# Kernel optimization log

Measured on AMD Instinct MI355X. Metric: run time of the kernel, lower is better.

## Reference

```python
import jax, jax.numpy as jnp
import numpy as np

NUM_HEADS = 8
NUM_GROUPS = 32
EPS = 1e-5


def setup_inputs() -> dict:
    key = jax.random.key(0)
    ks = jax.random.split(key, 7)
    B, C, H, W = 8, 512, 32, 32
    x = jax.random.normal(ks[0], (B, C, H, W), dtype=jnp.float32)
    # GroupNorm affine params
    gn_w = jnp.ones((C,), dtype=jnp.float32)
    gn_b = jnp.zeros((C,), dtype=jnp.float32)
    # 1x1 conv == linear over channel dim; store squeezed weights (out, in)
    qkv_w = jax.random.normal(ks[1], (3 * C, C), dtype=jnp.float32) * (1.0 / np.sqrt(C))
    qkv_b = jnp.zeros((3 * C,), dtype=jnp.float32)
    proj_w = jax.random.normal(ks[2], (C, C), dtype=jnp.float32) * (1.0 / np.sqrt(C))
    proj_b = jnp.zeros((C,), dtype=jnp.float32)
    return {"x": x, "gn_w": gn_w, "gn_b": gn_b, "qkv_w": qkv_w,
            "qkv_b": qkv_b, "proj_w": proj_w, "proj_b": proj_b}


def reference(x, gn_w, gn_b, qkv_w, qkv_b, proj_w, proj_b):
    B, C, H, W = x.shape
    G = NUM_GROUPS
    hd = C // NUM_HEADS
    scale = hd ** -0.5
    # GroupNorm: normalize over (C//G, H, W) per group
    xg = x.reshape(B, G, C // G, H, W)
    mean = xg.mean(axis=(2, 3, 4), keepdims=True)
    var = xg.var(axis=(2, 3, 4), keepdims=True)
    xn = ((xg - mean) * jax.lax.rsqrt(var + EPS)).reshape(B, C, H, W)
    xn = xn * gn_w[None, :, None, None] + gn_b[None, :, None, None]
    # QKV 1x1 conv
    qkv = jnp.einsum('bchw,oc->bohw', xn, qkv_w) + qkv_b[None, :, None, None]
    # (B, 3, heads, head_dim, HW) -> (3, B, heads, HW, head_dim)
    qkv = qkv.reshape(B, 3, NUM_HEADS, hd, H * W).transpose(1, 0, 2, 4, 3)
    q, k, v = qkv[0], qkv[1], qkv[2]
    attn = jax.nn.softmax(jnp.einsum('bhqd,bhkd->bhqk', q, k) * scale, axis=-1)
    out = jnp.einsum('bhqk,bhkd->bhqd', attn, v)  # (B, heads, HW, hd)
    out = out.transpose(0, 1, 3, 2).reshape(B, C, H, W)
    out = jnp.einsum('bchw,oc->bohw', out, proj_w) + proj_b[None, :, None, None]
    return out + x
```

## Files before the change

### kernel.cpp

```cpp
#include <hip/hip_runtime.h>
#include <hip/hip_bf16.h>
#include <math.h>

typedef __bf16 bf16_t;
typedef __bf16 bf16x8 __attribute__((ext_vector_type(8)));
typedef __bf16 bf16x4 __attribute__((ext_vector_type(4)));
typedef float  f32x4  __attribute__((ext_vector_type(4)));

#define NB    8
#define NC    512
#define NHW   1024
#define NHEAD 8
#define NHD   64
#define NG    32
#define NCG   16
#define NO3   1536

__device__ __forceinline__ void lds_load16(bf16_t* lds, const bf16_t* g) {
  __builtin_amdgcn_global_load_lds(
      (__attribute__((address_space(1))) unsigned int*)(g),
      (__attribute__((address_space(3))) unsigned int*)(void*)(lds),
      16, 0, 0);
}

__device__ __forceinline__ float sum16(float v) {
  v += __shfl_xor(v, 1); v += __shfl_xor(v, 2);
  v += __shfl_xor(v, 4); v += __shfl_xor(v, 8);
  return v;
}
__device__ __forceinline__ float max16(float v) {
  v = fmaxf(v, __shfl_xor(v, 1)); v = fmaxf(v, __shfl_xor(v, 2));
  v = fmaxf(v, __shfl_xor(v, 4)); v = fmaxf(v, __shfl_xor(v, 8));
  return v;
}

__global__ __launch_bounds__(256)
void gn_kernel(const float* __restrict__ x, const float* __restrict__ gw,
               const float* __restrict__ gb, bf16_t* __restrict__ xn)
{
  const int bg = blockIdx.x;
  const int b = bg >> 5, g = bg & 31;
  const float* xp = x + ((size_t)b * NC + g * NCG) * NHW;
  const int tid = threadIdx.x;
  const int wave = tid >> 6, lane = tid & 63;

  float s1 = 0.f, s2 = 0.f;
  const float4* xp4 = (const float4*)xp;
  for (int i = tid; i < 4096; i += 256) {
    float4 v = xp4[i];
    s1 += v.x + v.y + v.z + v.w;
    s2 += v.x * v.x + v.y * v.y + v.z * v.z + v.w * v.w;
  }
  for (int off = 32; off > 0; off >>= 1) {
    s1 += __shfl_down(s1, off);
    s2 += __shfl_down(s2, off);
  }
  __shared__ float red[16];
  if (lane == 0) { red[wave] = s1; red[8 + wave] = s2; }
  __syncthreads();
  float tot1 = red[0] + red[1] + red[2] + red[3];
  float tot2 = red[8] + red[9] + red[10] + red[11];
  const float mean = tot1 * (1.0f / 16384.0f);
  const float var  = tot2 * (1.0f / 16384.0f) - mean * mean;
  const float rstd = rsqrtf(var + 1e-5f);

  float gam[NCG], bet[NCG];
  #pragma unroll
  for (int c = 0; c < NCG; ++c) {
    gam[c] = gw[g * NCG + c] * rstd;
    bet[c] = gb[g * NCG + c] - mean * gam[c];
  }
  bf16_t* op = xn + (size_t)b * NHW * NC + g * NCG;
  for (int s = tid; s < NHW; s += 256) {
    __align__(16) bf16_t vals[NCG];
    #pragma unroll
    for (int c = 0; c < NCG; ++c)
      vals[c] = (bf16_t)(xp[c * NHW + s] * gam[c] + bet[c]);
    *(bf16x8*)(op + (size_t)s * NC)     = *(const bf16x8*)&vals[0];
    *(bf16x8*)(op + (size_t)s * NC + 8) = *(const bf16x8*)&vals[8];
  }
}

__global__ __launch_bounds__(256)
void wconv_kernel(const float* __restrict__ qw, const float* __restrict__ pw,
                  bf16_t* __restrict__ qwb, bf16_t* __restrict__ pwb)
{
  const int gid = blockIdx.x * 256 + threadIdx.x;
  const int n1 = NO3 * NC / 4;
  float4 v; bf16x4 o;
  if (gid < n1) {
    v = ((const float4*)qw)[gid];
    o[0] = (bf16_t)v.x; o[1] = (bf16_t)v.y; o[2] = (bf16_t)v.z; o[3] = (bf16_t)v.w;
    ((bf16x4*)qwb)[gid] = o;
  } else {
    int g2 = gid - n1;
    v = ((const float4*)pw)[g2];
    o[0] = (bf16_t)v.x; o[1] = (bf16_t)v.y; o[2] = (bf16_t)v.z; o[3] = (bf16_t)v.w;
    ((bf16x4*)pwb)[g2] = o;
  }
}

__device__ __forceinline__ void gemm_mainloop(const bf16_t* Ap, const bf16_t* Bp,
                                              bf16_t* sA, bf16_t* sB, f32x4 (&acc)[4][4])
{
  const int tid = threadIdx.x;
  const int wave = tid >> 6, lane = tid & 63;
  const int quad = lane >> 4, l16 = lane & 15;
  const int wm = wave >> 1, wn = wave & 1;
  for (int k0 = 0; k0 < 512; k0 += 32) {
    #pragma unroll
    for (int j = 0; j < 2; ++j) {
      int c = wave * 64 + j * 256 + lane;
      int row = c >> 2, ko = (c & 3) * 8;
      lds_load16(sA + (size_t)(wave * 64 + j * 256) * 8, Ap + (size_t)row * 512 + k0 + ko);
      lds_load16(sB + (size_t)(wave * 64 + j * 256) * 8, Bp + (size_t)row * 512 + k0 + ko);
    }
    __syncthreads();
    bf16x8 af[4], bfr[4];
    #pragma unroll
    for (int mi = 0; mi < 4; ++mi)
      af[mi] = *(const bf16x8*)(sA + (wm * 64 + mi * 16 + l16) * 32 + quad * 8);
    #pragma unroll
    for (int ni = 0; ni < 4; ++ni)
      bfr[ni] = *(const bf16x8*)(sB + (wn * 64 + ni * 16 + l16) * 32 + quad * 8);
    #pragma unroll
    for (int mi = 0; mi < 4; ++mi)
      #pragma unroll
      for (int ni = 0; ni < 4; ++ni)
        acc[mi][ni] = __builtin_amdgcn_mfma_f32_16x16x32_bf16(af[mi], bfr[ni], acc[mi][ni], 0, 0, 0);
    __syncthreads();
  }
}

__global__ __launch_bounds__(256, 2)
void qkv_gemm(const bf16_t* __restrict__ xn, const bf16_t* __restrict__ w,
              const float* __restrict__ bias,
              bf16_t* __restrict__ qbuf, bf16_t* __restrict__ kbuf, bf16_t* __restrict__ vbuf)
{
  __shared__ __align__(16) bf16_t smem[128 * 136];
  bf16_t* sA = smem;
  bf16_t* sB = smem + 4096;
  const int tid = threadIdx.x;
  const int wave = tid >> 6, lane = tid & 63;
  const int quad = lane >> 4, l16 = lane & 15;
  const int wm = wave >> 1, wn = wave & 1;
  const int bx = blockIdx.x, by = blockIdx.y, b = blockIdx.z;

  const bf16_t* Ap = xn + ((size_t)b * NHW + by * 128) * NC;
  const bf16_t* Bp = w + (size_t)bx * 128 * NC;
  f32x4 acc[4][4] = {};
  gemm_mainloop(Ap, Bp, sA, sB, acc);

  const int obase = bx * 128 + wn * 64;
  const int sbase = by * 128 + wm * 64;
  float bv[4];
  #pragma unroll
  for (int ni = 0; ni < 4; ++ni) bv[ni] = bias[obase + ni * 16 + l16];

  if (bx < 8) {
    const bool isq = (bx < 4);
    bf16_t* basep = isq ? qbuf : kbuf;
    const float scale = isq ? 0.125f : 1.0f;
    #pragma unroll
    for (int ni = 0; ni < 4; ++ni) {
      int o = obase + ni * 16 + l16;
      int hh = (o >> 6) & 7, dd = o & 63;
      bf16_t* dst = basep + ((size_t)(b * NHEAD + hh) * NHW) * NHD + dd;
      #pragma unroll
      for (int mi = 0; mi < 4; ++mi)
        #pragma unroll
        for (int r = 0; r < 4; ++r) {
          int s = sbase + mi * 16 + quad * 4 + r;
          dst[(size_t)s * NHD] = (bf16_t)((acc[mi][ni][r] + bv[ni]) * scale);
        }
    }
  } else {
    bf16_t* sC = smem;
    #pragma unroll
    for (int ni = 0; ni < 4; ++ni)
      #pragma unroll
      for (int mi = 0; mi < 4; ++mi)
        #pragma unroll
        for (int r = 0; r < 4; ++r)
          sC[(wn * 64 + ni * 16 + l16) * 136 + wm * 64 + mi * 16 + quad * 4 + r] =
              (bf16_t)(acc[mi][ni][r] + bv[ni]);
    __syncthreads();
    int o_local = tid >> 1, shalf = (tid & 1) << 6;
    int ov = (bx - 8) * 128 + o_local;
    int hh = ov >> 6, dd = ov & 63;
    bf16_t* dst = vbuf + ((size_t)(b * NHEAD + hh) * NHD + dd) * NHW + by * 128 + shalf;
    #pragma unroll
    for (int jj = 0; jj < 8; ++jj)
      *(bf16x8*)(dst + jj * 8) = *(const bf16x8*)&sC[o_local * 136 + shalf + jj * 8];
  }
}

__global__ __launch_bounds__(256, 2)
void attn_kernel(const bf16_t* __restrict__ qbuf, const bf16_t* __restrict__ kbuf,
                 const bf16_t* __restrict__ vbuf, bf16_t* __restrict__ obuf)
{
  __shared__ __align__(16) bf16_t Ks[128 * 72];
  __shared__ __align__(16) bf16_t Vs[64 * 136];
  __shared__ __align__(16) bf16_t Ps[4][32 * 136];

  const int tid = threadIdx.x;
  const int wave = tid >> 6, lane = tid & 63;
  const int quad = lane >> 4, l16 = lane & 15;
  const int idx = blockIdx.x;
  const int qt = idx & 7, h = (idx >> 3) & 7, b = idx >> 6;
  const size_t bh = (size_t)b * NHEAD + h;
  const bf16_t* qp = qbuf + (bh * NHW + qt * 128) * NHD;
  const bf16_t* kp = kbuf + bh * NHW * NHD;
  const bf16_t* vp = vbuf + bh * NHD * NHW;

  bf16x8 qf[2][2];
  #pragma unroll
  for (int mi = 0; mi < 2; ++mi)
    #pragma unroll
    for (int kc = 0; kc < 2; ++kc)
      qf[mi][kc] = *(const bf16x8*)(qp + (size_t)(wave * 32 + mi * 16 + l16) * NHD + kc * 32 + quad * 8);

  float m_i[2][4], l_i[2][4];
  f32x4 oacc[2][4] = {};
  #pragma unroll
  for (int mi = 0; mi < 2; ++mi)
    #pragma unroll
    for (int r = 0; r < 4; ++r) { m_i[mi][r] = -1e30f; l_i[mi][r] = 0.f; }

  for (int kt = 0; kt < 8; ++kt) {
    const bf16_t* ksrc = kp + (size_t)kt * 128 * NHD;
    const bf16_t* vsrc = vp + kt * 128;
    #pragma unroll
    for (int j = 0; j < 4; ++j) {
      int c = tid + j * 256;
      int t = c >> 3, doff = (c & 7) * 8;
      *(bf16x8*)&Ks[t * 72 + doff] = *(const bf16x8*)(ksrc + (size_t)t * NHD + doff);
    }
    #pragma unroll
    for (int j = 0; j < 4; ++j) {
      int c = tid + j * 256;
      int d = c >> 4, toff = (c & 15) * 8;
      *(bf16x8*)&Vs[d * 136 + toff] = *(const bf16x8*)(vsrc + (size_t)d * NHW + toff);
    }
    __syncthreads();

    f32x4 sf[2][8] = {};
    #pragma unroll
    for (int ni = 0; ni < 8; ++ni) {
      bf16x8 k0 = *(const bf16x8*)&Ks[(ni * 16 + l16) * 72 + quad * 8];
      bf16x8 k1 = *(const bf16x8*)&Ks[(ni * 16 + l16) * 72 + 32 + quad * 8];
      #pragma unroll
      for (int mi = 0; mi < 2; ++mi) {
        sf[mi][ni] = __builtin_amdgcn_mfma_f32_16x16x32_bf16(qf[mi][0], k0, sf[mi][ni], 0, 0, 0);
        sf[mi][ni] = __builtin_amdgcn_mfma_f32_16x16x32_bf16(qf[mi][1], k1, sf[mi][ni], 0, 0, 0);
      }
    }
    float alpha[2][4], rs[2][4];
    #pragma unroll
    for (int mi = 0; mi < 2; ++mi)
      #pragma unroll
      for (int r = 0; r < 4; ++r) {
        float mx = sf[mi][0][r];
        #pragma unroll
        for (int ni = 1; ni < 8; ++ni) mx = fmaxf(mx, sf[mi][ni][r]);
        mx = max16(mx);
        float mnew = fmaxf(m_i[mi][r], mx);
        alpha[mi][r] = __expf(m_i[mi][r] - mnew);
        m_i[mi][r] = mnew;
        rs[mi][r] = 0.f;
      }
    #pragma unroll
    for (int mi = 0; mi < 2; ++mi)
      #pragma unroll
      for (int ni = 0; ni < 8; ++ni)
        #pragma unroll
        for (int r = 0; r < 4; ++r) {
          float p = __expf(sf[mi][ni][r] - m_i[mi][r]);
          rs[mi][r] += p;
          Ps[wave][(mi * 16 + quad * 4 + r) * 136 + ni * 16 + l16] = (bf16_t)p;
        }
    #pragma unroll
    for (int mi = 0; mi < 2; ++mi)
      #pragma unroll
      for (int r = 0; r < 4; ++r)
        l_i[mi][r] = l_i[mi][r] * alpha[mi][r] + sum16(rs[mi][r]);
    #pragma unroll
    for (int mi = 0; mi < 2; ++mi)
      #pragma unroll
      for (int ni = 0; ni < 4; ++ni)
        #pragma unroll
        for (int r = 0; r < 4; ++r)
          oacc[mi][ni][r] *= alpha[mi][r];

    asm volatile("s_waitcnt lgkmcnt(0)" ::: "memory");

    #pragma unroll
    for (int kc = 0; kc < 4; ++kc) {
      bf16x8 pa0 = *(const bf16x8*)&Ps[wave][(l16) * 136 + kc * 32 + quad * 8];
      bf16x8 pa1 = *(const bf16x8*)&Ps[wave][(16 + l16) * 136 + kc * 32 + quad * 8];
      #pragma unroll
      for (int ni = 0; ni < 4; ++ni) {
        bf16x8 vf = *(const bf16x8*)&Vs[(ni * 16 + l16) * 136 + kc * 32 + quad * 8];
        oacc[0][ni] = __builtin_amdgcn_mfma_f32_16x16x32_bf16(pa0, vf, oacc[0][ni], 0, 0, 0);
        oacc[1][ni] = __builtin_amdgcn_mfma_f32_16x16x32_bf16(pa1, vf, oacc[1][ni], 0, 0, 0);
      }
    }
    __syncthreads();
  }

  #pragma unroll
  for (int mi = 0; mi < 2; ++mi)
    #pragma unroll
    for (int r = 0; r < 4; ++r) {
      float inv = 1.0f / l_i[mi][r];
      int s = qt * 128 + wave * 32 + mi * 16 + quad * 4 + r;
      bf16_t* orow = obuf + ((size_t)b * NHW + s) * NC + h * NHD;
      #pragma unroll
      for (int ni = 0; ni < 4; ++ni)
        orow[ni * 16 + l16] = (bf16_t)(oacc[mi][ni][r] * inv);
    }
}

__global__ __launch_bounds__(256, 2)
void proj_gemm(const bf16_t* __restrict__ ob, const bf16_t* __restrict__ w,
               const float* __restrict__ bias, const float* __restrict__ x,
               float* __restrict__ out)
{
  __shared__ __align__(16) bf16_t smem[8192];
  bf16_t* sA = smem;
  bf16_t* sB = smem + 4096;
  const int tid = threadIdx.x;
  const int wave = tid >> 6, lane = tid & 63;
  const int quad = lane >> 4, l16 = lane & 15;
  const int wm = wave >> 1, wn = wave & 1;
  const int bx = blockIdx.x, by = blockIdx.y, b = blockIdx.z;

  const bf16_t* Ap = w + (size_t)by * 128 * NC;
  const bf16_t* Bp = ob + ((size_t)b * NHW + bx * 128) * NC;
  f32x4 acc[4][4] = {};
  gemm_mainloop(Ap, Bp, sA, sB, acc);

  const int cobase = by * 128 + wm * 64;
  const int sbase  = bx * 128 + wn * 64;
  #pragma unroll
  for (int mi = 0; mi < 4; ++mi)
    #pragma unroll
    for (int r = 0; r < 4; ++r) {
      int co = cobase + mi * 16 + quad * 4 + r;
      float pb = bias[co];
      const float* xrow = x + ((size_t)b * NC + co) * NHW;
      float* orow = out + ((size_t)b * NC + co) * NHW;
      #pragma unroll
      for (int ni = 0; ni < 4; ++ni) {
        int s = sbase + ni * 16 + l16;
        orow[s] = acc[mi][ni][r] + pb + xrow[s];
      }
    }
}

extern "C" void kernel_launch(void* const* d_in, const int* in_sizes, int n_in,
                              void* d_out, int out_size, void* d_ws, size_t ws_size,
                              hipStream_t stream)
{
  const float* x      = (const float*)d_in[0];
  const float* gn_w   = (const float*)d_in[1];
  const float* gn_b   = (const float*)d_in[2];
  const float* qkv_w  = (const float*)d_in[3];
  const float* qkv_b  = (const float*)d_in[4];
  const float* proj_w = (const float*)d_in[5];
  const float* proj_b = (const float*)d_in[6];
  float* out = (float*)d_out;

  char* ws = (char*)d_ws;
  bf16_t* xn   = (bf16_t*)(ws);
  bf16_t* qwb  = (bf16_t*)(ws + 8388608);
  bf16_t* pwb  = (bf16_t*)(ws + 9961472);
  bf16_t* qbuf = (bf16_t*)(ws + 10485760);
  bf16_t* kbuf = (bf16_t*)(ws + 18874368);
  bf16_t* vbuf = (bf16_t*)(ws + 27262976);
  bf16_t* obuf = xn;

  gn_kernel<<<dim3(NB * NG), dim3(256), 0, stream>>>(x, gn_w, gn_b, xn);
  wconv_kernel<<<dim3(1024), dim3(256), 0, stream>>>(qkv_w, proj_w, qwb, pwb);
  qkv_gemm<<<dim3(12, 8, NB), dim3(256), 0, stream>>>(xn, qwb, qkv_b, qbuf, kbuf, vbuf);
  attn_kernel<<<dim3(512), dim3(256), 0, stream>>>(qbuf, kbuf, vbuf, obuf);
  proj_gemm<<<dim3(8, 4, NB), dim3(256), 0, stream>>>(obuf, pwb, proj_b, x, out);
}
```

Measured before the change: 177.3 us.

## Shrink attention tiles to 64 queries and 64 keys for more blocks and occupancy

The attention kernel now gives each wave 16 query rows instead of 32 and streams keys and values in 64-wide tiles instead of 128-wide. The grid doubles to 1024 blocks and launch bounds ask for 4 blocks per CU. Smaller register and LDS footprints should raise occupancy and spread the work over more blocks on the large CU count. The cost is more K/V reloads per block (each KV tile is loaded by twice as many blocks), more barriers per block, and less MFMA work per sync. A __syncthreads is also added before the LDS reuse in the QKV gemm's V-store path, likely to fix a race.

```diff
diff --git a/kernel.cpp b/kernel.cpp
--- a/kernel.cpp
+++ b/kernel.cpp
@@ -176,6 +176,7 @@
     }
   } else {
     bf16_t* sC = smem;
+    __syncthreads();
     #pragma unroll
     for (int ni = 0; ni < 4; ++ni)
       #pragma unroll
@@ -195,130 +196,109 @@
   }
 }
 
-__global__ __launch_bounds__(256, 2)
+__global__ __launch_bounds__(256, 4)
 void attn_kernel(const bf16_t* __restrict__ qbuf, const bf16_t* __restrict__ kbuf,
                  const bf16_t* __restrict__ vbuf, bf16_t* __restrict__ obuf)
 {
-  __shared__ __align__(16) bf16_t Ks[128 * 72];
-  __shared__ __align__(16) bf16_t Vs[64 * 136];
-  __shared__ __align__(16) bf16_t Ps[4][32 * 136];
+  __shared__ __align__(16) bf16_t Ks[64 * 72];
+  __shared__ __align__(16) bf16_t Vs[64 * 72];
+  __shared__ __align__(16) bf16_t Ps[4][16 * 72];
 
   const int tid = threadIdx.x;
   const int wave = tid >> 6, lane = tid & 63;
   const int quad = lane >> 4, l16 = lane & 15;
   const int idx = blockIdx.x;
-  const int qt = idx & 7, h = (idx >> 3) & 7, b = idx >> 6;
+  const int qt = idx & 15, h = (idx >> 4) & 7, b = idx >> 7;
   const size_t bh = (size_t)b * NHEAD + h;
-  const bf16_t* qp = qbuf + (bh * NHW + qt * 128) * NHD;
+  const bf16_t* qp = qbuf + (bh * NHW + qt * 64) * NHD;
   const bf16_t* kp = kbuf + bh * NHW * NHD;
   const bf16_t* vp = vbuf + bh * NHD * NHW;
 
-  bf16x8 qf[2][2];
-  #pragma unroll
-  for (int mi = 0; mi < 2; ++mi)
-    #pragma unroll
-    for (int kc = 0; kc < 2; ++kc)
-      qf[mi][kc] = *(const bf16x8*)(qp + (size_t)(wave * 32 + mi * 16 + l16) * NHD + kc * 32 + quad * 8);
-
-  float m_i[2][4], l_i[2][4];
-  f32x4 oacc[2][4] = {};
-  #pragma unroll
-  for (int mi = 0; mi < 2; ++mi)
-    #pragma unroll
-    for (int r = 0; r < 4; ++r) { m_i[mi][r] = -1e30f; l_i[mi][r] = 0.f; }
-
-  for (int kt = 0; kt < 8; ++kt) {
-    const bf16_t* ksrc = kp + (size_t)kt * 128 * NHD;
-    const bf16_t* vsrc = vp + kt * 128;
-    #pragma unroll
-    for (int j = 0; j < 4; ++j) {
+  bf16x8 qf[2];
+  #pragma unroll
+  for (int kc = 0; kc < 2; ++kc)
+    qf[kc] = *(const bf16x8*)(qp + (size_t)(wave * 16 + l16) * NHD + kc * 32 + quad * 8);
+
+  float m_i[4], l_i[4];
+  f32x4 oacc[4] = {};
+  #pragma unroll
+  for (int r = 0; r < 4; ++r) { m_i[r] = -1e30f; l_i[r] = 0.f; }
+
+  for (int kt = 0; kt < 16; ++kt) {
+    const bf16_t* ksrc = kp + (size_t)kt * 64 * NHD;
+    const bf16_t* vsrc = vp + kt * 64;
+    #pragma unroll
+    for (int j = 0; j < 2; ++j) {
       int c = tid + j * 256;
       int t = c >> 3, doff = (c & 7) * 8;
       *(bf16x8*)&Ks[t * 72 + doff] = *(const bf16x8*)(ksrc + (size_t)t * NHD + doff);
     }
     #pragma unroll
-    for (int j = 0; j < 4; ++j) {
+    for (int j = 0; j < 2; ++j) {
       int c = tid + j * 256;
-      int d = c >> 4, toff = (c & 15) * 8;
-      *(bf16x8*)&Vs[d * 136 + toff] = *(const bf16x8*)(vsrc + (size_t)d * NHW + toff);
-    }
-    __syncthreads();
-
-    f32x4 sf[2][8] = {};
-    #pragma unroll
-    for (int ni = 0; ni < 8; ++ni) {
+      int d = c >> 3, toff = (c & 7) * 8;
+      *(bf16x8*)&Vs[d * 72 + toff] = *(const bf16x8*)(vsrc + (size_t)d * NHW + toff);
+    }
+    __syncthreads();
+
+    f32x4 sf[4] = {};
+    #pragma unroll
+    for (int ni = 0; ni < 4; ++ni) {
       bf16x8 k0 = *(const bf16x8*)&Ks[(ni * 16 + l16) * 72 + quad * 8];
       bf16x8 k1 = *(const bf16x8*)&Ks[(ni * 16 + l16) * 72 + 32 + quad * 8];
-      #pragma unroll
-      for (int mi = 0; mi < 2; ++mi) {
-        sf[mi][ni] = __builtin_amdgcn_mfma_f32_16x16x32_bf16(qf[mi][0], k0, sf[mi][ni], 0, 0, 0);
-        sf[mi][ni] = __builtin_amdgcn_mfma_f32_16x16x32_bf16(qf[mi][1], k1, sf[mi][ni], 0, 0, 0);
+      sf[ni] = __builtin_amdgcn_mfma_f32_16x16x32_bf16(qf[0], k0, sf[ni], 0, 0, 0);
+      sf[ni] = __builtin_amdgcn_mfma_f32_16x16x32_bf16(qf[1], k1, sf[ni], 0, 0, 0);
+    }
+    float alpha[4], rs[4];
+    #pragma unroll
+    for (int r = 0; r < 4; ++r) {
+      float mx = fmaxf(fmaxf(sf[0][r], sf[1][r]), fmaxf(sf[2][r], sf[3][r]));
+      mx = max16(mx);
+      float mnew = fmaxf(m_i[r], mx);
+      alpha[r] = __expf(m_i[r] - mnew);
+      m_i[r] = mnew;
+      rs[r] = 0.f;
+    }
+    #pragma unroll
+    for (int ni = 0; ni < 4; ++ni)
+      #pragma unroll
+      for (int r = 0; r < 4; ++r) {
+        float p = __expf(sf[ni][r] - m_i[r]);
+        rs[r] += p;
+        Ps[wave][(quad * 4 + r) * 72 + ni * 16 + l16] = (bf16_t)p;
       }
-    }
-    float alpha[2][4], rs[2][4];
-    #pragma unroll
-    for (int mi = 0; mi < 2; ++mi)
-      #pragma unroll
-      for (int r = 0; r < 4; ++r) {
-        float mx = sf[mi][0][r];
-        #pragma unroll
-        for (int ni = 1; ni < 8; ++ni) mx = fmaxf(mx, sf[mi][ni][r]);
-        mx = max16(mx);
-        float mnew = fmaxf(m_i[mi][r], mx);
-        alpha[mi][r] = __expf(m_i[mi][r] - mnew);
-        m_i[mi][r] = mnew;
-        rs[mi][r] = 0.f;
+    #pragma unroll
+    for (int r = 0; r < 4; ++r)
+      l_i[r] = l_i[r] * alpha[r] + sum16(rs[r]);
+    #pragma unroll
+    for (int ni = 0; ni < 4; ++ni)
+      #pragma unroll
+      for (int r = 0; r < 4; ++r)
+        oacc[ni][r] *= alpha[r];
+
+    asm volatile("s_waitcnt lgkmcnt(0)" ::: "memory");
+
+    #pragma unroll
+    for (int kc = 0; kc < 2; ++kc) {
+      bf16x8 pa = *(const bf16x8*)&Ps[wave][l16 * 72 + kc * 32 + quad * 8];
+      #pragma unroll
+      for (int ni = 0; ni < 4; ++ni) {
+        bf16x8 vf = *(const bf16x8*)&Vs[(ni * 16 + l16) * 72 + kc * 32 + quad * 8];
+        oacc[ni] = __builtin_amdgcn_mfma_f32_16x16x32_bf16(pa, vf, oacc[ni], 0, 0, 0);
       }
-    #pragma unroll
-    for (int mi = 0; mi < 2; ++mi)
-      #pragma unroll
-      for (int ni = 0; ni < 8; ++ni)
-        #pragma unroll
-        for (int r = 0; r < 4; ++r) {
-          float p = __expf(sf[mi][ni][r] - m_i[mi][r]);
-          rs[mi][r] += p;
-          Ps[wave][(mi * 16 + quad * 4 + r) * 136 + ni * 16 + l16] = (bf16_t)p;
-        }
-    #pragma unroll
-    for (int mi = 0; mi < 2; ++mi)
-      #pragma unroll
-      for (int r = 0; r < 4; ++r)
-        l_i[mi][r] = l_i[mi][r] * alpha[mi][r] + sum16(rs[mi][r]);
-    #pragma unroll
-    for (int mi = 0; mi < 2; ++mi)
-      #pragma unroll
-      for (int ni = 0; ni < 4; ++ni)
-        #pragma unroll
-        for (int r = 0; r < 4; ++r)
-          oacc[mi][ni][r] *= alpha[mi][r];
-
-    asm volatile("s_waitcnt lgkmcnt(0)" ::: "memory");
-
-    #pragma unroll
-    for (int kc = 0; kc < 4; ++kc) {
-      bf16x8 pa0 = *(const bf16x8*)&Ps[wave][(l16) * 136 + kc * 32 + quad * 8];
-      bf16x8 pa1 = *(const bf16x8*)&Ps[wave][(16 + l16) * 136 + kc * 32 + quad * 8];
-      #pragma unroll
-      for (int ni = 0; ni < 4; ++ni) {
-        bf16x8 vf = *(const bf16x8*)&Vs[(ni * 16 + l16) * 136 + kc * 32 + quad * 8];
-        oacc[0][ni] = __builtin_amdgcn_mfma_f32_16x16x32_bf16(pa0, vf, oacc[0][ni], 0, 0, 0);
-        oacc[1][ni] = __builtin_amdgcn_mfma_f32_16x16x32_bf16(pa1, vf, oacc[1][ni], 0, 0, 0);
-      }
-    }
-    __syncthreads();
-  }
-
-  #pragma unroll
-  for (int mi = 0; mi < 2; ++mi)
-    #pragma unroll
-    for (int r = 0; r < 4; ++r) {
-      float inv = 1.0f / l_i[mi][r];
-      int s = qt * 128 + wave * 32 + mi * 16 + quad * 4 + r;
-      bf16_t* orow = obuf + ((size_t)b * NHW + s) * NC + h * NHD;
-      #pragma unroll
-      for (int ni = 0; ni < 4; ++ni)
-        orow[ni * 16 + l16] = (bf16_t)(oacc[mi][ni][r] * inv);
-    }
+    }
+    __syncthreads();
+  }
+
+  #pragma unroll
+  for (int r = 0; r < 4; ++r) {
+    float inv = 1.0f / l_i[r];
+    int s = qt * 64 + wave * 16 + quad * 4 + r;
+    bf16_t* orow = obuf + ((size_t)b * NHW + s) * NC + h * NHD;
+    #pragma unroll
+    for (int ni = 0; ni < 4; ++ni)
+      orow[ni * 16 + l16] = (bf16_t)(oacc[ni][r] * inv);
+  }
 }
 
 __global__ __launch_bounds__(256, 2)
@@ -383,6 +363,6 @@
   gn_kernel<<<dim3(NB * NG), dim3(256), 0, stream>>>(x, gn_w, gn_b, xn);
   wconv_kernel<<<dim3(1024), dim3(256), 0, stream>>>(qkv_w, proj_w, qwb, pwb);
   qkv_gemm<<<dim3(12, 8, NB), dim3(256), 0, stream>>>(xn, qwb, qkv_b, qbuf, kbuf, vbuf);
-  attn_kernel<<<dim3(512), dim3(256), 0, stream>>>(qbuf, kbuf, vbuf, obuf);
+  attn_kernel<<<dim3(1024), dim3(256), 0, stream>>>(qbuf, kbuf, vbuf, obuf);
   proj_gemm<<<dim3(8, 4, NB), dim3(256), 0, stream>>>(obuf, pwb, proj_b, x, out);
 }
```

Result: slower. 186.1 us (+4.9%).

## Compute transposed S^T in attention to keep P in registers, drop LDS staging

Applied to the files above, without the earlier changes.

The attention kernel now computes S^T = K·Q^T, so each lane holds scores for one query row. Softmax reductions become two cross-quad shuffles instead of per-row 16-lane shuffle trees. P feeds the PV MFMA straight from registers through 16x16x16 bf16 MFMAs, which removes the per-wave Ps shared-memory buffer, its writes and reads, and the lgkmcnt wait. It also adds a barrier before the QKV kernel's V-path shared-memory reuse, and uses smaller-K MFMAs for the PV product in exchange for dropping the LDS round trip.

```diff
diff --git a/kernel.cpp b/kernel.cpp
--- a/kernel.cpp
+++ b/kernel.cpp
@@ -6,6 +6,7 @@
 typedef __bf16 bf16x8 __attribute__((ext_vector_type(8)));
 typedef __bf16 bf16x4 __attribute__((ext_vector_type(4)));
 typedef float  f32x4  __attribute__((ext_vector_type(4)));
+typedef short  short4v __attribute__((ext_vector_type(4)));
 
 #define NB    8
 #define NC    512
@@ -23,15 +24,16 @@
       16, 0, 0);
 }
 
-__device__ __forceinline__ float sum16(float v) {
-  v += __shfl_xor(v, 1); v += __shfl_xor(v, 2);
-  v += __shfl_xor(v, 4); v += __shfl_xor(v, 8);
-  return v;
-}
-__device__ __forceinline__ float max16(float v) {
-  v = fmaxf(v, __shfl_xor(v, 1)); v = fmaxf(v, __shfl_xor(v, 2));
-  v = fmaxf(v, __shfl_xor(v, 4)); v = fmaxf(v, __shfl_xor(v, 8));
-  return v;
+__device__ __forceinline__ f32x4 mfma16(bf16x4 a, bf16x4 b, f32x4 c) {
+#if __has_builtin(__builtin_amdgcn_mfma_f32_16x16x16bf16_1k)
+  return __builtin_amdgcn_mfma_f32_16x16x16bf16_1k(
+      __builtin_bit_cast(short4v, a), __builtin_bit_cast(short4v, b), c, 0, 0, 0);
+#else
+  f32x4 d;
+  asm("v_mfma_f32_16x16x16_bf16 %0, %1, %2, %3"
+      : "=v"(d) : "v"(a), "v"(b), "v"(c));
+  return d;
+#endif
 }
 
 __global__ __launch_bounds__(256)
@@ -176,6 +178,7 @@
     }
   } else {
     bf16_t* sC = smem;
+    __syncthreads();
     #pragma unroll
     for (int ni = 0; ni < 4; ++ni)
       #pragma unroll
@@ -201,7 +204,6 @@
 {
   __shared__ __align__(16) bf16_t Ks[128 * 72];
   __shared__ __align__(16) bf16_t Vs[64 * 136];
-  __shared__ __align__(16) bf16_t Ps[4][32 * 136];
 
   const int tid = threadIdx.x;
   const int wave = tid >> 6, lane = tid & 63;
@@ -209,23 +211,19 @@
   const int idx = blockIdx.x;
   const int qt = idx & 7, h = (idx >> 3) & 7, b = idx >> 6;
   const size_t bh = (size_t)b * NHEAD + h;
-  const bf16_t* qp = qbuf + (bh * NHW + qt * 128) * NHD;
+  const bf16_t* qp = qbuf + (bh * NHW + qt * 128 + wave * 32) * NHD;
   const bf16_t* kp = kbuf + bh * NHW * NHD;
   const bf16_t* vp = vbuf + bh * NHD * NHW;
 
   bf16x8 qf[2][2];
   #pragma unroll
-  for (int mi = 0; mi < 2; ++mi)
+  for (int stile = 0; stile < 2; ++stile)
     #pragma unroll
     for (int kc = 0; kc < 2; ++kc)
-      qf[mi][kc] = *(const bf16x8*)(qp + (size_t)(wave * 32 + mi * 16 + l16) * NHD + kc * 32 + quad * 8);
-
-  float m_i[2][4], l_i[2][4];
-  f32x4 oacc[2][4] = {};
-  #pragma unroll
-  for (int mi = 0; mi < 2; ++mi)
-    #pragma unroll
-    for (int r = 0; r < 4; ++r) { m_i[mi][r] = -1e30f; l_i[mi][r] = 0.f; }
+      qf[stile][kc] = *(const bf16x8*)(qp + (size_t)(stile * 16 + l16) * NHD + kc * 32 + quad * 8);
+
+  float m_i[2] = {-1e30f, -1e30f}, l_i[2] = {0.f, 0.f};
+  f32x4 oacc[4][2] = {};
 
   for (int kt = 0; kt < 8; ++kt) {
     const bf16_t* ksrc = kp + (size_t)kt * 128 * NHD;
@@ -244,81 +242,84 @@
     }
     __syncthreads();
 
-    f32x4 sf[2][8] = {};
-    #pragma unroll
-    for (int ni = 0; ni < 8; ++ni) {
-      bf16x8 k0 = *(const bf16x8*)&Ks[(ni * 16 + l16) * 72 + quad * 8];
-      bf16x8 k1 = *(const bf16x8*)&Ks[(ni * 16 + l16) * 72 + 32 + quad * 8];
-      #pragma unroll
-      for (int mi = 0; mi < 2; ++mi) {
-        sf[mi][ni] = __builtin_amdgcn_mfma_f32_16x16x32_bf16(qf[mi][0], k0, sf[mi][ni], 0, 0, 0);
-        sf[mi][ni] = __builtin_amdgcn_mfma_f32_16x16x32_bf16(qf[mi][1], k1, sf[mi][ni], 0, 0, 0);
+    f32x4 st[2][8];
+    #pragma unroll
+    for (int mt = 0; mt < 8; ++mt) {
+      bf16x8 ka0 = *(const bf16x8*)&Ks[(mt * 16 + l16) * 72 + quad * 8];
+      bf16x8 ka1 = *(const bf16x8*)&Ks[(mt * 16 + l16) * 72 + 32 + quad * 8];
+      #pragma unroll
+      for (int stile = 0; stile < 2; ++stile) {
+        f32x4 z = {};
+        z = __builtin_amdgcn_mfma_f32_16x16x32_bf16(ka0, qf[stile][0], z, 0, 0, 0);
+        z = __builtin_amdgcn_mfma_f32_16x16x32_bf16(ka1, qf[stile][1], z, 0, 0, 0);
+        st[stile][mt] = z;
       }
     }
-    float alpha[2][4], rs[2][4];
-    #pragma unroll
-    for (int mi = 0; mi < 2; ++mi)
-      #pragma unroll
-      for (int r = 0; r < 4; ++r) {
-        float mx = sf[mi][0][r];
-        #pragma unroll
-        for (int ni = 1; ni < 8; ++ni) mx = fmaxf(mx, sf[mi][ni][r]);
-        mx = max16(mx);
-        float mnew = fmaxf(m_i[mi][r], mx);
-        alpha[mi][r] = __expf(m_i[mi][r] - mnew);
-        m_i[mi][r] = mnew;
-        rs[mi][r] = 0.f;
+
+    #pragma unroll
+    for (int stile = 0; stile < 2; ++stile) {
+      float mx = -1e30f;
+      #pragma unroll
+      for (int mt = 0; mt < 8; ++mt)
+        #pragma unroll
+        for (int r = 0; r < 4; ++r) mx = fmaxf(mx, st[stile][mt][r]);
+      mx = fmaxf(mx, __shfl_xor(mx, 16));
+      mx = fmaxf(mx, __shfl_xor(mx, 32));
+      float mnew = fmaxf(m_i[stile], mx);
+      float alpha = __expf(m_i[stile] - mnew);
+      m_i[stile] = mnew;
+      float rs = 0.f;
+      #pragma unroll
+      for (int mt = 0; mt < 8; ++mt)
+        #pragma unroll
+        for (int r = 0; r < 4; ++r) {
+          float p = __expf(st[stile][mt][r] - mnew);
+          rs += p;
+          st[stile][mt][r] = p;
+        }
+      rs += __shfl_xor(rs, 16);
+      rs += __shfl_xor(rs, 32);
+      l_i[stile] = l_i[stile] * alpha + rs;
+      #pragma unroll
+      for (int mi = 0; mi < 4; ++mi)
+        #pragma unroll
+        for (int r = 0; r < 4; ++r)
+          oacc[mi][stile][r] *= alpha;
+    }
+
+    #pragma unroll
+    for (int mt = 0; mt < 8; ++mt) {
+      bf16x4 pb[2];
+      #pragma unroll
+      for (int stile = 0; stile < 2; ++stile) {
+        pb[stile][0] = (bf16_t)st[stile][mt][0];
+        pb[stile][1] = (bf16_t)st[stile][mt][1];
+        pb[stile][2] = (bf16_t)st[stile][mt][2];
+        pb[stile][3] = (bf16_t)st[stile][mt][3];
       }
-    #pragma unroll
-    for (int mi = 0; mi < 2; ++mi)
-      #pragma unroll
-      for (int ni = 0; ni < 8; ++ni)
-        #pragma unroll
-        for (int r = 0; r < 4; ++r) {
-          float p = __expf(sf[mi][ni][r] - m_i[mi][r]);
-          rs[mi][r] += p;
-          Ps[wave][(mi * 16 + quad * 4 + r) * 136 + ni * 16 + l16] = (bf16_t)p;
-        }
-    #pragma unroll
-    for (int mi = 0; mi < 2; ++mi)
-      #pragma unroll
-      for (int r = 0; r < 4; ++r)
-        l_i[mi][r] = l_i[mi][r] * alpha[mi][r] + sum16(rs[mi][r]);
-    #pragma unroll
-    for (int mi = 0; mi < 2; ++mi)
-      #pragma unroll
-      for (int ni = 0; ni < 4; ++ni)
-        #pragma unroll
-        for (int r = 0; r < 4; ++r)
-          oacc[mi][ni][r] *= alpha[mi][r];
-
-    asm volatile("s_waitcnt lgkmcnt(0)" ::: "memory");
-
-    #pragma unroll
-    for (int kc = 0; kc < 4; ++kc) {
-      bf16x8 pa0 = *(const bf16x8*)&Ps[wave][(l16) * 136 + kc * 32 + quad * 8];
-      bf16x8 pa1 = *(const bf16x8*)&Ps[wave][(16 + l16) * 136 + kc * 32 + quad * 8];
-      #pragma unroll
-      for (int ni = 0; ni < 4; ++ni) {
-        bf16x8 vf = *(const bf16x8*)&Vs[(ni * 16 + l16) * 136 + kc * 32 + quad * 8];
-        oacc[0][ni] = __builtin_amdgcn_mfma_f32_16x16x32_bf16(pa0, vf, oacc[0][ni], 0, 0, 0);
-        oacc[1][ni] = __builtin_amdgcn_mfma_f32_16x16x32_bf16(pa1, vf, oacc[1][ni], 0, 0, 0);
+      #pragma unroll
+      for (int mi = 0; mi < 4; ++mi) {
+        bf16x4 va = *(const bf16x4*)&Vs[(mi * 16 + l16) * 136 + mt * 16 + quad * 4];
+        oacc[mi][0] = mfma16(va, pb[0], oacc[mi][0]);
+        oacc[mi][1] = mfma16(va, pb[1], oacc[mi][1]);
       }
     }
     __syncthreads();
   }
 
   #pragma unroll
-  for (int mi = 0; mi < 2; ++mi)
-    #pragma unroll
-    for (int r = 0; r < 4; ++r) {
-      float inv = 1.0f / l_i[mi][r];
-      int s = qt * 128 + wave * 32 + mi * 16 + quad * 4 + r;
-      bf16_t* orow = obuf + ((size_t)b * NHW + s) * NC + h * NHD;
-      #pragma unroll
-      for (int ni = 0; ni < 4; ++ni)
-        orow[ni * 16 + l16] = (bf16_t)(oacc[mi][ni][r] * inv);
-    }
+  for (int stile = 0; stile < 2; ++stile) {
+    float inv = 1.0f / l_i[stile];
+    int s = qt * 128 + wave * 32 + stile * 16 + l16;
+    bf16_t* orow = obuf + ((size_t)b * NHW + s) * NC + h * NHD;
+    #pragma unroll
+    for (int mi = 0; mi < 4; ++mi) {
+      __align__(8) bf16_t o4[4];
+      #pragma unroll
+      for (int r = 0; r < 4; ++r) o4[r] = (bf16_t)(oacc[mi][stile][r] * inv);
+      *(bf16x4*)(orow + mi * 16 + quad * 4) = *(const bf16x4*)o4;
+    }
+  }
 }
 
 __global__ __launch_bounds__(256, 2)
```

Measured after the change: 172.4 us. 1.03x faster.
